# Kernel optimization log

Measured on AMD Instinct MI355X. Metric: run time of the kernel, lower is better.

The kernel has to match this reference:

```python
import jax, jax.numpy as jnp
from jax import lax
import numpy as np

PAD = 0
V, DW, H, T, B = 30000, 512, 512, 50, 128


def _xavier(key, shape):
    fan_in, fan_out = shape[1], shape[0]
    lim = float(np.sqrt(6.0 / (fan_in + fan_out)))
    return jax.random.uniform(key, shape, jnp.float32, -lim, lim)


def setup_inputs() -> dict:
    key = jax.random.key(0)
    ks = jax.random.split(key, 8)
    return {
        "user": jax.random.randint(ks[0], (B,), 0, 10000),
        "item": jax.random.randint(ks[1], (B,), 0, 10000),
        "review_input": jax.random.randint(ks[2], (T, B), 0, V),
        "review_target": jax.random.randint(ks[3], (T, B), 0, V),
        "word_emb": jax.random.normal(ks[4], (V, DW), jnp.float32) * 0.02,
        "W_ih": _xavier(ks[5], (3 * H, DW)),
        "W_hh": _xavier(ks[6], (3 * H, H)),
        "b_ih": jnp.zeros((3 * H,), jnp.float32),
        "b_hh": jnp.zeros((3 * H,), jnp.float32),
        "W_out": _xavier(ks[7], (V, H)),
        "b_out": jnp.zeros((V,), jnp.float32),
    }


def reference(user, item, review_input, review_target,
              word_emb, W_ih, W_hh, b_ih, b_hh, W_out, b_out):
    n_batch = user.shape[0]
    # embed all timesteps at once: [T, B, DW]
    x = word_emb[review_input]
    # precompute input-to-gate projections: [T, B, 3H]
    xg = jnp.einsum('tbd,gd->tbg', x, W_ih) + b_ih
    h0 = jnp.zeros((n_batch, H), x.dtype)

    def step(h, xg_t):
        hg = h @ W_hh.T + b_hh                      # [B, 3H]
        xr, xz, xn = jnp.split(xg_t, 3, axis=-1)    # PyTorch order: r, z, n
        hr, hz, hn = jnp.split(hg, 3, axis=-1)
        r = jax.nn.sigmoid(xr + hr)
        z = jax.nn.sigmoid(xz + hz)
        n = jnp.tanh(xn + r * hn)
        h_new = (1.0 - z) * n + z * h
        return h_new, h_new

    _, outs = lax.scan(step, h0, xg)                # [T, B, H]
    logits = outs.reshape(-1, H) @ W_out.T + b_out  # [T*B, V]
    tgt = review_target.reshape(-1)
    logp = jax.nn.log_softmax(logits, axis=-1)
    nll = -jnp.take_along_axis(logp, tgt[:, None], axis=1)[:, 0]
    mask = tgt != PAD
    out_loss = jnp.where(mask, nll, 0.0)            # F.cross_entropy reduction='none', ignore_index=PAD
    denom = jnp.maximum(jnp.sum(mask), 1).astype(out_loss.dtype)
    obj = jnp.sum(out_loss) / denom                 # mean over non-ignored tokens
    return out_loss, obj
```

## Files before the change

### kernel.cpp

```cpp
#include <hip/hip_runtime.h>

typedef short short8 __attribute__((ext_vector_type(8)));
typedef float f32x4 __attribute__((ext_vector_type(4)));
typedef float f4 __attribute__((ext_vector_type(4)));
typedef unsigned short ushort_t;

#define VOCAB 30000
#define DW 512
#define KDIM 512
#define HDIM 512
#define G3 1536
#define TT 50
#define BB 128
#define M_ROWS 6400
#define NPAD 30208
#define NT2 472

__device__ __forceinline__ float b2f(ushort_t u){ return __uint_as_float(((unsigned)u)<<16); }
__device__ __forceinline__ ushort_t f2b(float f){
    unsigned u = __float_as_uint(f);
    unsigned r = (u + 0x7fffu + ((u>>16)&1u)) >> 16;
    return (ushort_t)r;
}
__device__ __forceinline__ float sigf(float x){
    float e = __expf(-x);
    return __builtin_amdgcn_rcpf(1.0f + e);
}
__device__ __forceinline__ float tanh_(float x){
    return 2.0f*sigf(2.0f*x) - 1.0f;
}
__device__ __forceinline__ void gload16(const ushort_t* g, char* l){
    __builtin_amdgcn_global_load_lds((const __attribute__((address_space(1))) void*)g,
                                     (__attribute__((address_space(3))) void*)l, 16, 0, 0);
}

__global__ void k_cvt4(const f4* __restrict__ s, ushort_t* __restrict__ d, int n4){
    int i = blockIdx.x*blockDim.x + threadIdx.x;
    if (i < n4){
        f4 v = s[i];
        unsigned lo = (unsigned)f2b(v[0]) | ((unsigned)f2b(v[1]) << 16);
        unsigned hi = (unsigned)f2b(v[2]) | ((unsigned)f2b(v[3]) << 16);
        *(uint2*)(d + (size_t)i*4) = make_uint2(lo, hi);
    }
}
__global__ void k_zero_u(ushort_t* __restrict__ d, int n){
    int i = blockIdx.x*blockDim.x + threadIdx.x;
    if (i < n) d[i] = 0;
}
__global__ void k_gather(const float* __restrict__ emb, const int* __restrict__ idx,
                         ushort_t* __restrict__ x){
    int row = blockIdx.x;
    int v = idx[row];
    const float2* src = (const float2*)(emb + (size_t)v*DW);
    unsigned* dst = (unsigned*)(x + (size_t)row*DW);
    for (int d = threadIdx.x; d < DW/2; d += blockDim.x){
        float2 w = src[d];
        dst[d] = (unsigned)f2b(w.x) | ((unsigned)f2b(w.y) << 16);
    }
}
__global__ void k_biasg(const float* __restrict__ bi, const float* __restrict__ bh,
                        float* __restrict__ bg, float* __restrict__ hf,
                        ushort_t* __restrict__ hb){
    int i = blockIdx.x*blockDim.x + threadIdx.x;
    if (i < G3) bg[i] = bi[i] + (i < 2*HDIM ? bh[i] : 0.0f);
    if (i < BB*HDIM){ hf[i] = 0.0f; hb[i] = 0; }
}

template<int MODE, int NBLK>
__global__ __launch_bounds__(256, 3) void k_gemm5(const ushort_t* __restrict__ A,
        const ushort_t* __restrict__ Bw, const float* __restrict__ bias,
        ushort_t* __restrict__ Cout, float* __restrict__ psum){
    __shared__ ushort_t As[128*32];
    __shared__ ushort_t Bs[128*32];
    const int nwg = NBLK * 50;
    const int q = nwg >> 3;
    int wgid = (blockIdx.x & 7)*q + (blockIdx.x >> 3);
    int band = wgid / (10*NBLK);
    int rr   = wgid % (10*NBLK);
    int nb = rr / 10;
    int mb = band*10 + (rr % 10);
    int n0 = nb*128, m0 = mb*128;

    int lane = threadIdx.x & 63, wv = threadIdx.x >> 6;
    int lo = lane & 15, hi = lane >> 4;
    int wr = wv >> 1, wc = wv & 1;
    f32x4 acc[4][4] = {};
    int xsl = ((lane & 3) ^ ((lane >> 3) & 3)) * 8;
    const ushort_t* gA = A  + (size_t)(m0 + wv*32 + (lane>>2))*KDIM + xsl;
    const ushort_t* gB = Bw + (size_t)(n0 + wv*32 + (lane>>2))*KDIM + xsl;
    char* lA = (char*)As + wv*2048;
    char* lB = (char*)Bs + wv*2048;
    int rchunk = (hi ^ ((lo >> 1) & 3)) * 8;
    for (int kt = 0; kt < 16; ++kt){
        __syncthreads();
        int k0 = kt*32;
        gload16(gA + k0,           lA);
        gload16(gA + 16*KDIM + k0, lA + 1024);
        gload16(gB + k0,           lB);
        gload16(gB + 16*KDIM + k0, lB + 1024);
        __syncthreads();
        short8 av[4], bv[4];
        #pragma unroll
        for (int mi = 0; mi < 4; ++mi)
            av[mi] = *(const short8*)&As[(wr*64 + mi*16 + lo)*32 + rchunk];
        #pragma unroll
        for (int ni = 0; ni < 4; ++ni)
            bv[ni] = *(const short8*)&Bs[(wc*64 + ni*16 + lo)*32 + rchunk];
        #pragma unroll
        for (int mi = 0; mi < 4; ++mi)
            #pragma unroll
            for (int ni = 0; ni < 4; ++ni)
                acc[mi][ni] = __builtin_amdgcn_mfma_f32_16x16x32_bf16(av[mi], bv[ni], acc[mi][ni], 0, 0, 0);
    }

    if (MODE == 0){
        #pragma unroll
        for (int ni = 0; ni < 4; ++ni){
            int n = n0 + wc*64 + ni*16 + lo;
            float bb = bias[n];
            #pragma unroll
            for (int mi = 0; mi < 4; ++mi){
                #pragma unroll
                for (int j = 0; j < 4; ++j){
                    int m = m0 + wr*64 + mi*16 + hi*4 + j;
                    Cout[(size_t)m*G3 + n] = f2b(acc[mi][ni][j] + bb);
                }
            }
        }
    } else {
        const int NT = NBLK*2;
        float bov[4];
        bool valid[4];
        #pragma unroll
        for (int ni = 0; ni < 4; ++ni){
            int col = n0 + wc*64 + ni*16 + lo;
            valid[ni] = (col < VOCAB);
            bov[ni] = valid[ni] ? bias[col] : 0.0f;
        }
        int tile = nb*2 + wc;
        #pragma unroll
        for (int mi = 0; mi < 4; ++mi){
            #pragma unroll
            for (int j = 0; j < 4; ++j){
                float s = 0.0f;
                #pragma unroll
                for (int ni = 0; ni < 4; ++ni)
                    s += valid[ni] ? __expf(acc[mi][ni][j] + bov[ni]) : 0.0f;
                for (int d = 1; d < 16; d <<= 1) s += __shfl_xor(s, d, 64);
                if (lo == 0){
                    int m = m0 + wr*64 + mi*16 + hi*4 + j;
                    psum[(size_t)m*NT + tile] = s;
                }
            }
        }
    }
}

__global__ __launch_bounds__(64) void k_step(const ushort_t* __restrict__ hprev_b,
        const float* __restrict__ hprev_f, const ushort_t* __restrict__ Whh,
        const ushort_t* __restrict__ xg, const float* __restrict__ bh,
        float* __restrict__ hnext_f, ushort_t* __restrict__ hnext_b,
        ushort_t* __restrict__ outs, int t){
    int lane = threadIdx.x;
    int lo = lane & 15, hi = lane >> 4;
    int c16 = blockIdx.x * 16;
    int b0  = blockIdx.y * 16;
    f32x4 acc[3] = {};
    const ushort_t* Arow = hprev_b + (size_t)(b0 + lo)*HDIM;
    #pragma unroll
    for (int kk = 0; kk < 16; ++kk){
        int k0 = kk*32 + hi*8;
        short8 a = *(const short8*)(Arow + k0);
        #pragma unroll
        for (int g = 0; g < 3; ++g){
            short8 b = *(const short8*)(Whh + (size_t)(g*HDIM + c16 + lo)*HDIM + k0);
            acc[g] = __builtin_amdgcn_mfma_f32_16x16x32_bf16(a, b, acc[g], 0, 0, 0);
        }
    }
    int c = c16 + lo;
    float bhn = bh[2*HDIM + c];
    const ushort_t* xgt = xg + (size_t)t*BB*G3;
    #pragma unroll
    for (int j = 0; j < 4; ++j){
        int bt = b0 + hi*4 + j;
        float xr = b2f(xgt[(size_t)bt*G3 + c]);
        float xz = b2f(xgt[(size_t)bt*G3 + HDIM + c]);
        float xn = b2f(xgt[(size_t)bt*G3 + 2*HDIM + c]);
        float r  = sigf(acc[0][j] + xr);
        float z  = sigf(acc[1][j] + xz);
        float n  = tanh_(xn + r*(acc[2][j] + bhn));
        float hold = hprev_f[(size_t)bt*HDIM + c];
        float hnew = (1.0f - z)*n + z*hold;
        hnext_f[(size_t)bt*HDIM + c] = hnew;
        ushort_t hb = f2b(hnew);
        hnext_b[(size_t)bt*HDIM + c] = hb;
        outs[((size_t)t*BB + bt)*HDIM + c] = hb;
    }
}

__global__ __launch_bounds__(256) void k_loss(const ushort_t* __restrict__ outs,
        const ushort_t* __restrict__ Wo, const float* __restrict__ bo,
        const float* __restrict__ psum, const int* __restrict__ tgt,
        float* __restrict__ out){
    int lane = threadIdx.x & 63, wv = threadIdx.x >> 6;
    int row = blockIdx.x*4 + wv;
    int tg = tgt[row];
    const float* ps = psum + (size_t)row*NT2;
    float S = 0.0f;
    for (int t = lane; t < NT2; t += 64) S += ps[t];
    for (int d = 1; d < 64; d <<= 1) S += __shfl_xor(S, d, 64);
    float lse = __logf(S);
    const ushort_t* a = outs + (size_t)row*HDIM + lane*8;
    const ushort_t* w = Wo + (size_t)tg*DW + lane*8;
    float s = 0.0f;
    #pragma unroll
    for (int j = 0; j < 8; ++j) s += b2f(a[j]) * b2f(w[j]);
    for (int d = 1; d < 64; d <<= 1) s += __shfl_xor(s, d, 64);
    if (lane == 0){
        float logit = s + bo[tg];
        out[row] = (tg != 0) ? (lse - logit) : 0.0f;
    }
}

__global__ __launch_bounds__(1024) void k_obj(const float* __restrict__ loss,
        const int* __restrict__ tgt, float* __restrict__ out){
    __shared__ float ss[1024];
    __shared__ int   sc[1024];
    float s = 0.0f; int c = 0;
    for (int i = threadIdx.x; i < M_ROWS; i += 1024){
        s += loss[i];
        c += (tgt[i] != 0) ? 1 : 0;
    }
    ss[threadIdx.x] = s; sc[threadIdx.x] = c;
    __syncthreads();
    for (int d = 512; d > 0; d >>= 1){
        if (threadIdx.x < (unsigned)d){ ss[threadIdx.x] += ss[threadIdx.x+d]; sc[threadIdx.x] += sc[threadIdx.x+d]; }
        __syncthreads();
    }
    if (threadIdx.x == 0) out[M_ROWS] = ss[0] / (float)(sc[0] > 0 ? sc[0] : 1);
}

extern "C" void kernel_launch(void* const* d_in, const int* in_sizes, int n_in,
                              void* d_out, int out_size, void* d_ws, size_t ws_size,
                              hipStream_t stream) {
    const int*   review_input  = (const int*)d_in[2];
    const int*   review_target = (const int*)d_in[3];
    const float* word_emb = (const float*)d_in[4];
    const float* W_ih = (const float*)d_in[5];
    const float* W_hh = (const float*)d_in[6];
    const float* b_ih = (const float*)d_in[7];
    const float* b_hh = (const float*)d_in[8];
    const float* W_out = (const float*)d_in[9];
    const float* b_out = (const float*)d_in[10];
    float* out = (float*)d_out;
    (void)n_in; (void)in_sizes; (void)out_size; (void)ws_size;

    char* ws = (char*)d_ws;
    size_t off = 0;
    auto alloc = [&](size_t bytes)->char*{
        char* p = ws + off;
        off = (off + bytes + 255) & ~(size_t)255;
        return p;
    };
    ushort_t* Wout_b = (ushort_t*)alloc((size_t)NPAD*DW*2);
    ushort_t* Wih_b  = (ushort_t*)alloc((size_t)G3*DW*2);
    ushort_t* Whh_b  = (ushort_t*)alloc((size_t)G3*HDIM*2);
    ushort_t* outs_b = (ushort_t*)alloc((size_t)M_ROWS*HDIM*2);
    float*    biasg  = (float*)alloc((size_t)G3*4);
    float*    h_f    = (float*)alloc((size_t)2*BB*HDIM*4);
    ushort_t* h_b    = (ushort_t*)alloc((size_t)2*BB*HDIM*2);
    ushort_t* xb     = (ushort_t*)alloc((size_t)M_ROWS*DW*2);
    ushort_t* xg     = (ushort_t*)alloc((size_t)M_ROWS*G3*2);
    float*    psum   = (float*)xb;

    k_cvt4<<<(G3*DW/4+255)/256, 256, 0, stream>>>((const f4*)W_ih, Wih_b, G3*DW/4);
    k_cvt4<<<(G3*HDIM/4+255)/256, 256, 0, stream>>>((const f4*)W_hh, Whh_b, G3*HDIM/4);
    k_cvt4<<<(VOCAB*DW/4+255)/256, 256, 0, stream>>>((const f4*)W_out, Wout_b, VOCAB*DW/4);
    k_zero_u<<<((NPAD-VOCAB)*DW+255)/256, 256, 0, stream>>>(Wout_b + (size_t)VOCAB*DW, (NPAD-VOCAB)*DW);
    k_gather<<<M_ROWS, 256, 0, stream>>>(word_emb, review_input, xb);
    k_biasg<<<(BB*HDIM+255)/256, 256, 0, stream>>>(b_ih, b_hh, biasg, h_f, h_b);

    k_gemm5<0, 12><<<600, 256, 0, stream>>>(xb, Wih_b, biasg, xg, nullptr);

    for (int t = 0; t < TT; ++t){
        int cur = t & 1, nxt = cur ^ 1;
        k_step<<<dim3(HDIM/16, BB/16), 64, 0, stream>>>(h_b + (size_t)cur*BB*HDIM,
                                       h_f + (size_t)cur*BB*HDIM,
                                       Whh_b, xg, b_hh,
                                       h_f + (size_t)nxt*BB*HDIM,
                                       h_b + (size_t)nxt*BB*HDIM,
                                       outs_b, t);
    }

    k_gemm5<1, 236><<<11800, 256, 0, stream>>>(outs_b, Wout_b, b_out, nullptr, psum);
    k_loss<<<M_ROWS/4, 256, 0, stream>>>(outs_b, Wout_b, b_out, psum, review_target, out);
    k_obj<<<1, 1024, 0, stream>>>(out, review_target, out);
}
```

Before: 510.5 us.

## Split GRU step K-reduction across four waves with LDS reduction

Each recurrent step block now uses four wavefronts, each computing a quarter of the K=512 dot products with MFMA. The partial accumulators are then summed through shared memory before the gate nonlinearity, which is now done one element per thread. The aim is to shorten the serial MFMA chain per step, which sits on the latency-bound critical path of 50 sequential launches. In exchange it adds a barrier and LDS traffic to every step.

Result: no change. 513.7 us (+0.6%).

```diff
diff --git a/kernel.cpp b/kernel.cpp
--- a/kernel.cpp
+++ b/kernel.cpp
@@ -156,46 +156,54 @@
     }
 }
 
-__global__ __launch_bounds__(64) void k_step(const ushort_t* __restrict__ hprev_b,
+__global__ __launch_bounds__(256) void k_step(const ushort_t* __restrict__ hprev_b,
         const float* __restrict__ hprev_f, const ushort_t* __restrict__ Whh,
         const ushort_t* __restrict__ xg, const float* __restrict__ bh,
         float* __restrict__ hnext_f, ushort_t* __restrict__ hnext_b,
         ushort_t* __restrict__ outs, int t){
-    int lane = threadIdx.x;
+    __shared__ float gl[3][4][16][17];
+    int tid = threadIdx.x;
+    int lane = tid & 63, wv = tid >> 6;
     int lo = lane & 15, hi = lane >> 4;
     int c16 = blockIdx.x * 16;
     int b0  = blockIdx.y * 16;
     f32x4 acc[3] = {};
-    const ushort_t* Arow = hprev_b + (size_t)(b0 + lo)*HDIM;
+    const ushort_t* Arow = hprev_b + (size_t)(b0 + lo)*HDIM + wv*128;
+    const ushort_t* Bbase = Whh + (size_t)(c16 + lo)*HDIM + wv*128;
     #pragma unroll
-    for (int kk = 0; kk < 16; ++kk){
+    for (int kk = 0; kk < 4; ++kk){
         int k0 = kk*32 + hi*8;
         short8 a = *(const short8*)(Arow + k0);
         #pragma unroll
         for (int g = 0; g < 3; ++g){
-            short8 b = *(const short8*)(Whh + (size_t)(g*HDIM + c16 + lo)*HDIM + k0);
+            short8 b = *(const short8*)(Bbase + (size_t)g*HDIM*HDIM + k0);
             acc[g] = __builtin_amdgcn_mfma_f32_16x16x32_bf16(a, b, acc[g], 0, 0, 0);
         }
     }
-    int c = c16 + lo;
-    float bhn = bh[2*HDIM + c];
-    const ushort_t* xgt = xg + (size_t)t*BB*G3;
     #pragma unroll
-    for (int j = 0; j < 4; ++j){
-        int bt = b0 + hi*4 + j;
-        float xr = b2f(xgt[(size_t)bt*G3 + c]);
-        float xz = b2f(xgt[(size_t)bt*G3 + HDIM + c]);
-        float xn = b2f(xgt[(size_t)bt*G3 + 2*HDIM + c]);
-        float r  = sigf(acc[0][j] + xr);
-        float z  = sigf(acc[1][j] + xz);
-        float n  = tanh_(xn + r*(acc[2][j] + bhn));
-        float hold = hprev_f[(size_t)bt*HDIM + c];
-        float hnew = (1.0f - z)*n + z*hold;
-        hnext_f[(size_t)bt*HDIM + c] = hnew;
-        ushort_t hb = f2b(hnew);
-        hnext_b[(size_t)bt*HDIM + c] = hb;
-        outs[((size_t)t*BB + bt)*HDIM + c] = hb;
-    }
+    for (int g = 0; g < 3; ++g)
+        #pragma unroll
+        for (int j = 0; j < 4; ++j)
+            gl[g][wv][hi*4 + j][lo] = acc[g][j];
+    __syncthreads();
+    int b = tid >> 4, c = tid & 15;
+    int bt = b0 + b, cc = c16 + c;
+    float hr = gl[0][0][b][c] + gl[0][1][b][c] + gl[0][2][b][c] + gl[0][3][b][c];
+    float hz = gl[1][0][b][c] + gl[1][1][b][c] + gl[1][2][b][c] + gl[1][3][b][c];
+    float hn = gl[2][0][b][c] + gl[2][1][b][c] + gl[2][2][b][c] + gl[2][3][b][c];
+    const ushort_t* xgt = xg + (size_t)t*BB*G3 + (size_t)bt*G3;
+    float xr = b2f(xgt[cc]);
+    float xz = b2f(xgt[HDIM + cc]);
+    float xn = b2f(xgt[2*HDIM + cc]);
+    float r  = sigf(hr + xr);
+    float z  = sigf(hz + xz);
+    float n  = tanh_(xn + r*(hn + bh[2*HDIM + cc]));
+    float hold = hprev_f[(size_t)bt*HDIM + cc];
+    float hnew = (1.0f - z)*n + z*hold;
+    hnext_f[(size_t)bt*HDIM + cc] = hnew;
+    ushort_t hv = f2b(hnew);
+    hnext_b[(size_t)bt*HDIM + cc] = hv;
+    outs[((size_t)t*BB + bt)*HDIM + cc] = hv;
 }
 
 __global__ __launch_bounds__(256) void k_loss(const ushort_t* __restrict__ outs,
@@ -284,7 +292,7 @@
 
     for (int t = 0; t < TT; ++t){
         int cur = t & 1, nxt = cur ^ 1;
-        k_step<<<dim3(HDIM/16, BB/16), 64, 0, stream>>>(h_b + (size_t)cur*BB*HDIM,
+        k_step<<<dim3(HDIM/16, BB/16), 256, 0, stream>>>(h_b + (size_t)cur*BB*HDIM,
                                        h_f + (size_t)cur*BB*HDIM,
                                        Whh_b, xg, b_hh,
                                        h_f + (size_t)nxt*BB*HDIM,
```
